# Kernel optimization log

Measured on AMD Instinct MI355X. Metric: run time of the kernel, lower is better.

Reference implementation:

```python
import jax, jax.numpy as jnp
import numpy as np

B, S, D, H, DFF, L, R, V = 2, 1024, 1024, 16, 4096, 2, 3, 32000
HD = D // H


def layer_norm(x, g, b, eps=1e-5):
    mu = jnp.mean(x, axis=-1, keepdims=True)
    var = jnp.var(x, axis=-1, keepdims=True)
    return (x - mu) / jnp.sqrt(var + eps) * g + b


def recursion_block(x, mask, Wqkv, bqkv, Wo, bo, W1, b1, W2, b2, ln1_g, ln1_b, ln2_g, ln2_b):
    # shared pre-LN transformer stack of L layers, applied once per recursion step
    Bc, Sc, _ = x.shape
    scale = 1.0 / np.sqrt(HD).astype(np.float32)
    for l in range(L):
        h = layer_norm(x, ln1_g[l], ln1_b[l])
        qkv = h @ Wqkv[l] + bqkv[l]
        q, k, v = jnp.split(qkv, 3, axis=-1)
        q = q.reshape(Bc, Sc, H, HD).transpose(0, 2, 1, 3)
        k = k.reshape(Bc, Sc, H, HD).transpose(0, 2, 1, 3)
        v = v.reshape(Bc, Sc, H, HD).transpose(0, 2, 1, 3)
        scores = jnp.einsum('bhqd,bhkd->bhqk', q, k) * scale + mask
        attn = jax.nn.softmax(scores, axis=-1)
        o = jnp.einsum('bhqk,bhkd->bhqd', attn, v).transpose(0, 2, 1, 3).reshape(Bc, Sc, D)
        x = x + o @ Wo[l] + bo[l]
        h2 = layer_norm(x, ln2_g[l], ln2_b[l])
        x = x + jax.nn.gelu(h2 @ W1[l] + b1[l]) @ W2[l] + b2[l]
    return x


def setup_inputs() -> dict:
    key = jax.random.key(0)
    ks = jax.random.split(key, 12)
    n = lambda k, shape: (jax.random.normal(k, shape, jnp.float32) * 0.02)
    return {
        'input_ids': jax.random.randint(ks[0], (B, S), 0, V),
        'token_embed': n(ks[1], (V, D)),
        'pos_embed': n(ks[2], (S, D)),
        'Wqkv': n(ks[3], (L, D, 3 * D)), 'bqkv': jnp.zeros((L, 3 * D), jnp.float32),
        'Wo': n(ks[4], (L, D, D)), 'bo': jnp.zeros((L, D), jnp.float32),
        'W1': n(ks[5], (L, D, DFF)), 'b1': jnp.zeros((L, DFF), jnp.float32),
        'W2': n(ks[6], (L, DFF, D)), 'b2': jnp.zeros((L, D), jnp.float32),
        'ln1_g': jnp.ones((L, D), jnp.float32), 'ln1_b': jnp.zeros((L, D), jnp.float32),
        'ln2_g': jnp.ones((L, D), jnp.float32), 'ln2_b': jnp.zeros((L, D), jnp.float32),
        'final_g': jnp.ones((D,), jnp.float32), 'final_b': jnp.zeros((D,), jnp.float32),
        'Wr': n(ks[7], (D, R)), 'br': jnp.zeros((R,), jnp.float32),
    }


def reference(input_ids, token_embed, pos_embed, Wqkv, bqkv, Wo, bo, W1, b1, W2, b2,
              ln1_g, ln1_b, ln2_g, ln2_b, final_g, final_b, Wr, br):
    h = token_embed[input_ids] + pos_embed[None, :, :]            # [B,S,D]
    mask = jnp.where(jnp.tril(jnp.ones((S, S), bool)), 0.0, -jnp.inf)[None, None]  # [1,1,S,S]
    # token-choice router on detached hidden states
    rlogits = jax.lax.stop_gradient(h) @ Wr + br                  # [B,S,R]
    probs = jax.nn.softmax(rlogits, axis=-1)
    depth_map = jnp.argmax(rlogits, axis=-1) + 1                  # depths in 1..R
    importance = probs.mean(axis=(0, 1))
    router_loss = R * jnp.sum(importance ** 2)                    # load-balance aux loss
    res = h
    for step in range(R):
        step_mask = depth_map >= step + 1                         # [B,S] bool
        upd = recursion_block(res, mask, Wqkv, bqkv, Wo, bo, W1, b1, W2, b2,
                              ln1_g, ln1_b, ln2_g, ln2_b)
        res = jnp.where(step_mask[..., None], upd, res)
    hf = layer_norm(res, final_g, final_b)
    logits = hf @ token_embed.T                                   # tied lm_head
    return logits, depth_map, router_loss
```

## Files before the change

kernel.cpp:

```cpp
#include <hip/hip_runtime.h>
#include <hip/hip_bf16.h>

#define DD 1024
#define SS 1024
#define BB 2
#define HH 16
#define DFFN 4096
#define LLAYERS 2
#define RSTEPS 3
#define VV 32000
#define NTOK (BB*SS)

typedef __attribute__((ext_vector_type(8))) short s16x8;
typedef __attribute__((ext_vector_type(8))) __bf16 bf16x8;
typedef __attribute__((ext_vector_type(4))) float f32x4;

__device__ __forceinline__ unsigned short f2bf(float f) {
  unsigned int u = __float_as_uint(f);
  u += 0x7FFFu + ((u >> 16) & 1u);
  return (unsigned short)(u >> 16);
}

__device__ __forceinline__ f32x4 mfma16(s16x8 a, s16x8 b, f32x4 c) {
  return __builtin_amdgcn_mfma_f32_16x16x32_bf16(
      __builtin_bit_cast(bf16x8, a), __builtin_bit_cast(bf16x8, b), c, 0, 0, 0);
}

__device__ __forceinline__ void gload16(const unsigned short* g, unsigned short* l) {
  __builtin_amdgcn_global_load_lds(
      (const __attribute__((address_space(1))) unsigned int*)(const void*)g,
      (__attribute__((address_space(3))) unsigned int*)(void*)l, 16, 0, 0);
}

#define BAR()  asm volatile("s_barrier" ::: "memory")
#define LGK0() do { asm volatile("s_waitcnt lgkmcnt(0)" ::: "memory"); \
                    __builtin_amdgcn_sched_barrier(0); } while (0)
#define VM4()  asm volatile("s_waitcnt vmcnt(4)" ::: "memory")
#define VM0()  asm volatile("s_waitcnt vmcnt(0)" ::: "memory")

__global__ __launch_bounds__(256) void wtrans_all_kernel(
    const float* __restrict__ Wqkv, const float* __restrict__ Wo,
    const float* __restrict__ W1, const float* __restrict__ W2,
    const float* __restrict__ te,
    unsigned short* __restrict__ WqkvT, unsigned short* __restrict__ WoT,
    unsigned short* __restrict__ W1T, unsigned short* __restrict__ W2T,
    unsigned short* __restrict__ teb) {
  const int bid = blockIdx.x;
  const int tid = threadIdx.x;
  if (bid >= 6144) {
    long i = ((long)(bid - 6144) * 256 + tid) * 8;
    float4 v0 = *(const float4*)(te + i);
    float4 v1 = *(const float4*)(te + i + 4);
    ushort4 a, b;
    a.x = f2bf(v0.x); a.y = f2bf(v0.y); a.z = f2bf(v0.z); a.w = f2bf(v0.w);
    b.x = f2bf(v1.x); b.y = f2bf(v1.y); b.z = f2bf(v1.z); b.w = f2bf(v1.w);
    *(ushort4*)(teb + i) = a;
    *(ushort4*)(teb + i + 4) = b;
    return;
  }
  const float* src; unsigned short* dst; int Kd, Nd, local;
  if (bid < 1536) {
    int l = (bid >= 768);
    local = bid - l * 768;
    src = Wqkv + (long)l * DD * 3 * DD; dst = WqkvT + (long)l * 3 * DD * DD;
    Kd = DD; Nd = 3 * DD;
  } else if (bid < 2048) {
    int l = (bid - 1536) >> 8; local = (bid - 1536) & 255;
    src = Wo + (long)l * DD * DD; dst = WoT + (long)l * DD * DD;
    Kd = DD; Nd = DD;
  } else if (bid < 4096) {
    int l = (bid - 2048) >> 10; local = (bid - 2048) & 1023;
    src = W1 + (long)l * DD * DFFN; dst = W1T + (long)l * DFFN * DD;
    Kd = DD; Nd = DFFN;
  } else {
    int l = (bid - 4096) >> 10; local = (bid - 4096) & 1023;
    src = W2 + (long)l * DFFN * DD; dst = W2T + (long)l * DD * DFFN;
    Kd = DFFN; Nd = DD;
  }
  const int tn = Nd >> 6;
  const int n0 = (local % tn) * 64, k0 = (local / tn) * 64;
  __shared__ unsigned short t[64][68];
#pragma unroll
  for (int c = 0; c < 4; ++c) {
    int p = tid + c * 256;
    int kr = p >> 4, nc = (p & 15) * 4;
    float4 v = *(const float4*)(src + (long)(k0 + kr) * Nd + n0 + nc);
    t[nc + 0][kr] = f2bf(v.x);
    t[nc + 1][kr] = f2bf(v.y);
    t[nc + 2][kr] = f2bf(v.z);
    t[nc + 3][kr] = f2bf(v.w);
  }
  __syncthreads();
#pragma unroll
  for (int c = 0; c < 4; ++c) {
    int p = tid + c * 256;
    int nr = p >> 4, kc = (p & 15) * 4;
    ushort4 o;
    o.x = t[nr][kc]; o.y = t[nr][kc + 1]; o.z = t[nr][kc + 2]; o.w = t[nr][kc + 3];
    *(ushort4*)(dst + (long)(n0 + nr) * Kd + k0 + kc) = o;
  }
}

__global__ __launch_bounds__(256) void embed_router_kernel(
    const int* __restrict__ ids, const float* __restrict__ te,
    const float* __restrict__ pe, const float* __restrict__ Wr,
    const float* __restrict__ br, float* __restrict__ res,
    float* __restrict__ probs, float* __restrict__ depth_ws,
    float* __restrict__ out_depth) {
  int row = blockIdx.x;
  int s = row & (SS - 1);
  int id = ids[row];
  int t = threadIdx.x;
  int d = t * 4;
  float4 a = *(const float4*)(te + (long)id * DD + d);
  float4 p = *(const float4*)(pe + (long)s * DD + d);
  float4 o; o.x = a.x + p.x; o.y = a.y + p.y; o.z = a.z + p.z; o.w = a.w + p.w;
  *(float4*)(res + (long)row * DD + d) = o;
  float a0 = 0.f, a1 = 0.f, a2 = 0.f;
  float hv[4] = {o.x, o.y, o.z, o.w};
#pragma unroll
  for (int j = 0; j < 4; ++j) {
    int dd = d + j;
    a0 += hv[j] * Wr[dd * 3 + 0];
    a1 += hv[j] * Wr[dd * 3 + 1];
    a2 += hv[j] * Wr[dd * 3 + 2];
  }
  for (int off = 32; off; off >>= 1) {
    a0 += __shfl_down(a0, off);
    a1 += __shfl_down(a1, off);
    a2 += __shfl_down(a2, off);
  }
  __shared__ float red[4][3];
  int wave = t >> 6;
  if ((t & 63) == 0) { red[wave][0] = a0; red[wave][1] = a1; red[wave][2] = a2; }
  __syncthreads();
  if (t == 0) {
    a0 = red[0][0] + red[1][0] + red[2][0] + red[3][0] + br[0];
    a1 = red[0][1] + red[1][1] + red[2][1] + red[3][1] + br[1];
    a2 = red[0][2] + red[1][2] + red[2][2] + red[3][2] + br[2];
    float m = fmaxf(a0, fmaxf(a1, a2));
    float e0 = expf(a0 - m), e1 = expf(a1 - m), e2 = expf(a2 - m);
    float inv = 1.f / (e0 + e1 + e2);
    probs[row * 3 + 0] = e0 * inv;
    probs[row * 3 + 1] = e1 * inv;
    probs[row * 3 + 2] = e2 * inv;
    int am = 0; float bv = a0;
    if (a1 > bv) { bv = a1; am = 1; }
    if (a2 > bv) { bv = a2; am = 2; }
    float dm = (float)(am + 1);
    depth_ws[row] = dm;
    out_depth[row] = dm;
  }
}

__global__ __launch_bounds__(256) void router_finalize_kernel(
    const float* __restrict__ probs, float* __restrict__ out_loss) {
  __shared__ float red[256][3];
  int t = threadIdx.x;
  float s0 = 0.f, s1 = 0.f, s2 = 0.f;
  for (int r = t; r < NTOK; r += 256) {
    s0 += probs[r * 3 + 0]; s1 += probs[r * 3 + 1]; s2 += probs[r * 3 + 2];
  }
  red[t][0] = s0; red[t][1] = s1; red[t][2] = s2;
  __syncthreads();
  for (int off = 128; off; off >>= 1) {
    if (t < off) {
      red[t][0] += red[t + off][0];
      red[t][1] += red[t + off][1];
      red[t][2] += red[t + off][2];
    }
    __syncthreads();
  }
  if (t == 0) {
    float i0 = red[0][0] / NTOK, i1 = red[0][1] / NTOK, i2 = red[0][2] / NTOK;
    out_loss[0] = (float)RSTEPS * (i0 * i0 + i1 * i1 + i2 * i2);
  }
}

__global__ __launch_bounds__(256) void ln_kernel(
    const float* __restrict__ x, const float* __restrict__ g,
    const float* __restrict__ b, unsigned short* __restrict__ y) {
  int row = blockIdx.x;
  int t = threadIdx.x;
  float4 v = *(const float4*)(x + (long)row * DD + t * 4);
  float s = v.x + v.y + v.z + v.w;
  float q = v.x * v.x + v.y * v.y + v.z * v.z + v.w * v.w;
  for (int off = 32; off; off >>= 1) {
    s += __shfl_down(s, off);
    q += __shfl_down(q, off);
  }
  __shared__ float rs[4], rq[4];
  int wave = t >> 6;
  if ((t & 63) == 0) { rs[wave] = s; rq[wave] = q; }
  __syncthreads();
  float S_ = rs[0] + rs[1] + rs[2] + rs[3];
  float Q_ = rq[0] + rq[1] + rq[2] + rq[3];
  float mu = S_ * (1.f / DD);
  float var = Q_ * (1.f / DD) - mu * mu;
  float rstd = rsqrtf(var + 1e-5f);
  int d = t * 4;
  float4 gg = *(const float4*)(g + d);
  float4 bb = *(const float4*)(b + d);
  ushort4 ov;
  ov.x = f2bf((v.x - mu) * rstd * gg.x + bb.x);
  ov.y = f2bf((v.y - mu) * rstd * gg.y + bb.y);
  ov.z = f2bf((v.z - mu) * rstd * gg.z + bb.z);
  ov.w = f2bf((v.w - mu) * rstd * gg.w + bb.w);
  *(ushort4*)(y + (long)row * DD + d) = ov;
}

__device__ __forceinline__ void stageA8(unsigned short* S, int buf, int qm,
    const unsigned short* A, int lda, long m0, int kt, int tid) {
  unsigned short* dst = S + buf * 32768 + qm * 8192;
#pragma unroll
  for (int c = 0; c < 2; ++c) {
    int idx = tid + c * 512;
    int L = (idx << 4) ^ (((idx >> 5) & 1) << 5);
    int band = L >> 13, row = (L >> 7) & 63, kel = (L & 127) >> 1;
    gload16(A + (m0 + band * 128 + qm * 64 + row) * (long)lda + kt * 64 + kel,
            dst + idx * 8);
  }
}

__device__ __forceinline__ void stageB8(unsigned short* S, int buf, int qn,
    const unsigned short* Bt, int ldb, long n0, int kt, int tid) {
  unsigned short* dst = S + buf * 32768 + 16384 + qn * 8192;
#pragma unroll
  for (int c = 0; c < 2; ++c) {
    int idx = tid + c * 512;
    int L = (idx << 4) ^ (((idx >> 5) & 1) << 5);
    int band = L >> 12, row = (L >> 7) & 31, kel = (L & 127) >> 1;
    gload16(Bt + (n0 + band * 64 + qn * 32 + row) * (long)ldb + kt * 64 + kel,
            dst + idx * 8);
  }
}

__device__ __forceinline__ void read_af8(const unsigned short* S, int base,
    int wm, int l16, int g, s16x8 af[2][4]) {
  const int swz = ((l16 >> 2) & 1) << 5;
#pragma unroll
  for (int kk = 0; kk < 2; ++kk)
#pragma unroll
    for (int mf = 0; mf < 4; ++mf) {
      int L = (wm * 8192 + (mf * 16 + l16) * 128 + (kk * 32 + g * 8) * 2) ^ swz;
      af[kk][mf] = *(const s16x8*)(S + base + (L >> 1));
    }
}

__device__ __forceinline__ void read_bf8(const unsigned short* S, int base,
    int wn, int l16, int g, s16x8 bf[2][2]) {
  const int swz = ((l16 >> 2) & 1) << 5;
#pragma unroll
  for (int kk = 0; kk < 2; ++kk)
#pragma unroll
    for (int nf = 0; nf < 2; ++nf) {
      int L = (wn * 4096 + (nf * 16 + l16) * 128 + (kk * 32 + g * 8) * 2) ^ swz;
      bf[kk][nf] = *(const s16x8*)(S + base + (L >> 1));
    }
}

template<int QM, int QN>
__device__ __forceinline__ void do_mfma8(f32x4 acc[8][4],
    const s16x8 af[2][4], const s16x8 bf[2][2]) {
  __builtin_amdgcn_s_setprio(1);
#pragma unroll
  for (int kk = 0; kk < 2; ++kk)
#pragma unroll
    for (int mf = 0; mf < 4; ++mf)
#pragma unroll
      for (int nf = 0; nf < 2; ++nf)
        acc[QM * 4 + mf][QN * 2 + nf] =
            mfma16(af[kk][mf], bf[kk][nf], acc[QM * 4 + mf][QN * 2 + nf]);
  __builtin_amdgcn_s_setprio(0);
}

template<int CBF16, int BIAS, int GELU_ACT>
__global__ __launch_bounds__(512, 1) void gemm256_kernel(
    const unsigned short* __restrict__ A, int lda,
    const unsigned short* __restrict__ Bt, int ldb,
    void* __restrict__ Cv, int ldc,
    const float* __restrict__ bias, int K, int Mblocks) {
  __shared__ unsigned short S[65536];
  const int tid = threadIdx.x;
  const int lane = tid & 63, wave = tid >> 6;
  const int g = lane >> 4, l16 = lane & 15;
  const int wm = wave >> 2, wn = wave & 3;
  const int nwg = gridDim.x * gridDim.y;
  const int orig = blockIdx.x + blockIdx.y * gridDim.x;
  const int q = nwg >> 3, r = nwg & 7;
  const int xcd = orig & 7, loc = orig >> 3;
  const int wgid = (xcd < r ? xcd * (q + 1) : r * (q + 1) + (xcd - r) * q) + loc;
  const long m0 = (long)(wgid % Mblocks) * 256;
  const long n0 = (long)(wgid / Mblocks) * 256;

  f32x4 acc[8][4] = {};
  s16x8 af[2][4], bf[2][2];
  const int NI = K >> 7;

  stageA8(S, 0, 0, A, lda, m0, 0, tid);
  stageA8(S, 0, 1, A, lda, m0, 0, tid);
  stageB8(S, 0, 0, Bt, ldb, n0, 0, tid);
  stageB8(S, 0, 1, Bt, ldb, n0, 0, tid);
  stageA8(S, 1, 0, A, lda, m0, 1, tid);
  stageB8(S, 1, 1, Bt, ldb, n0, 1, tid);
  VM4(); BAR();

  for (int i = 0; i < NI; ++i) {
    const int kt1 = 2 * i + 1, kt2 = 2 * i + 2, kt3 = 2 * i + 3;
    const bool more = (i + 1 < NI);
    read_af8(S, 0, wm, l16, g, af);
    read_bf8(S, 16384, wn, l16, g, bf);
    stageA8(S, 1, 1, A, lda, m0, kt1, tid);
    BAR(); LGK0();
    do_mfma8<0, 0>(acc, af, bf);
    BAR();
    read_bf8(S, 16384 + 8192, wn, l16, g, bf);
    stageB8(S, 1, 0, Bt, ldb, n0, kt1, tid);
    BAR(); LGK0();
    do_mfma8<0, 1>(acc, af, bf);
    BAR();
    read_af8(S, 8192, wm, l16, g, af);
    if (more) stageA8(S, 0, 0, A, lda, m0, kt2, tid);
    BAR(); LGK0();
    do_mfma8<1, 1>(acc, af, bf);
    BAR();
    read_bf8(S, 16384, wn, l16, g, bf);
    if (more) stageB8(S, 0, 1, Bt, ldb, n0, kt2, tid);
    BAR(); LGK0();
    do_mfma8<1, 0>(acc, af, bf);
    if (more) { VM4(); } else { VM0(); }
    BAR();
    read_af8(S, 32768, wm, l16, g, af);
    read_bf8(S, 32768 + 16384, wn, l16, g, bf);
    if (more) stageA8(S, 0, 1, A, lda, m0, kt2, tid);
    BAR(); LGK0();
    do_mfma8<0, 0>(acc, af, bf);
    BAR();
    read_bf8(S, 32768 + 16384 + 8192, wn, l16, g, bf);
    if (more) stageB8(S, 0, 0, Bt, ldb, n0, kt2, tid);
    BAR(); LGK0();
    do_mfma8<0, 1>(acc, af, bf);
    BAR();
    read_af8(S, 32768 + 8192, wm, l16, g, af);
    if (more) stageA8(S, 1, 0, A, lda, m0, kt3, tid);
    BAR(); LGK0();
    do_mfma8<1, 1>(acc, af, bf);
    BAR();
    read_bf8(S, 32768 + 16384, wn, l16, g, bf);
    if (more) stageB8(S, 1, 1, Bt, ldb, n0, kt3, tid);
    BAR(); LGK0();
    do_mfma8<1, 0>(acc, af, bf);
    VM4(); BAR();
  }

#pragma unroll
  for (int mf = 0; mf < 8; ++mf) {
#pragma unroll
    for (int nf = 0; nf < 4; ++nf) {
      long row0 = m0 + wm * 128 + mf * 16 + g * 4;
      long col = n0 + wn * 64 + nf * 16 + l16;
      float bv = BIAS ? bias[col] : 0.f;
#pragma unroll
      for (int rr = 0; rr < 4; ++rr) {
        float v = acc[mf][nf][rr] + bv;
        if (GELU_ACT) {
          float x3 = v * v * v;
          v = 0.5f * v * (1.f + tanhf(0.7978845608028654f * (v + 0.044715f * x3)));
        }
        if (CBF16) ((unsigned short*)Cv)[(row0 + rr) * (long)ldc + col] = f2bf(v);
        else       ((float*)Cv)[(row0 + rr) * (long)ldc + col] = v;
      }
    }
  }
}

template<int BN, int CBF16, int BIAS, int RESID, int GELU_ACT, int SELW, int QKVW>
__global__ __launch_bounds__(256) void gemm128_kernel(
    const unsigned short* __restrict__ A, int lda,
    const unsigned short* __restrict__ Bt, int ldb,
    void* __restrict__ Cv, int ldc,
    const float* __restrict__ bias,
    const float* __restrict__ resid, int ldr,
    const float* __restrict__ depth_ws, float stepf,
    unsigned short* __restrict__ vtw,
    int K) {
  constexpr int BM = 128;
  constexpr int WN = BN / 2;
  constexpr int MR = 4;
  constexpr int NR = WN / 16;
  __shared__ unsigned short As[BM * 64];
  __shared__ unsigned short Bs[BN * 64];
  const int tid = threadIdx.x;
  const int lane = tid & 63, wave = tid >> 6;
  const int g = lane >> 4, l16 = lane & 15;
  const int wr = wave >> 1, wc = wave & 1;
  int lin = blockIdx.x + blockIdx.y * gridDim.x;
  int per = (gridDim.x * gridDim.y) >> 3;
  int v = (lin & 7) * per + (lin >> 3);
  const long m0 = (long)(v % gridDim.y) * BM;
  const long n0 = (long)(v / gridDim.y) * BN;
  f32x4 acc[MR][NR] = {};
  for (int k0 = 0; k0 < K; k0 += 64) {
    __syncthreads();
#pragma unroll
    for (int c = 0; c < BM / 32; ++c) {
      int p = tid + c * 256;
      int r = p >> 3, kq = (p & 7) * 8;
      gload16(A + (m0 + r) * (long)lda + k0 + kq, &As[p * 8]);
    }
#pragma unroll
    for (int c = 0; c < BN / 32; ++c) {
      int p = tid + c * 256;
      int r = p >> 3, kq = (p & 7) * 8;
      gload16(Bt + (n0 + r) * (long)ldb + k0 + kq, &Bs[p * 8]);
    }
    __syncthreads();
#pragma unroll
    for (int kk = 0; kk < 2; ++kk) {
      s16x8 af[MR], bf[NR];
#pragma unroll
      for (int m = 0; m < MR; ++m)
        af[m] = *(const s16x8*)&As[(wr * 64 + m * 16 + l16) * 64 + kk * 32 + g * 8];
#pragma unroll
      for (int n = 0; n < NR; ++n)
        bf[n] = *(const s16x8*)&Bs[(wc * WN + n * 16 + l16) * 64 + kk * 32 + g * 8];
#pragma unroll
      for (int m = 0; m < MR; ++m)
#pragma unroll
        for (int n = 0; n < NR; ++n)
          acc[m][n] = mfma16(af[m], bf[n], acc[m][n]);
    }
  }
  const bool vblk = QKVW && (n0 >= 2048);
#pragma unroll
  for (int m = 0; m < MR; ++m) {
#pragma unroll
    for (int n = 0; n < NR; ++n) {
      long row_base = m0 + wr * 64 + m * 16 + g * 4;
      long col = n0 + wc * WN + n * 16 + l16;
      float bv = BIAS ? bias[col] : 0.f;
      float vv4[4];
#pragma unroll
      for (int r = 0; r < 4; ++r) {
        long row = row_base + r;
        float vv = acc[m][n][r] + bv;
        if (RESID) vv += resid[row * (long)ldr + col];
        if (GELU_ACT) {
          float x3 = vv * vv * vv;
          vv = 0.5f * vv * (1.f + tanhf(0.7978845608028654f * (vv + 0.044715f * x3)));
        }
        vv4[r] = vv;
      }
      if (QKVW && vblk) {
        int rel = (int)col - 2048;
        int h = rel >> 6, d = rel & 63;
        int b = (int)(row_base >> 10);
        int s = (int)(row_base & 1023);
        ushort4 o;
        o.x = f2bf(vv4[0]); o.y = f2bf(vv4[1]);
        o.z = f2bf(vv4[2]); o.w = f2bf(vv4[3]);
        *(ushort4*)(vtw + (((long)(b * 16 + h) * 64 + d) * SS + s)) = o;
      } else {
#pragma unroll
        for (int r = 0; r < 4; ++r) {
          long row = row_base + r;
          if (SELW) {
            if (depth_ws[row] >= stepf)
              ((float*)Cv)[row * (long)ldc + col] = vv4[r];
          } else if (CBF16) {
            ((unsigned short*)Cv)[row * (long)ldc + col] = f2bf(vv4[r]);
          } else {
            ((float*)Cv)[row * (long)ldc + col] = vv4[r];
          }
        }
      }
    }
  }
}

__global__ __launch_bounds__(512) void attn_kernel(
    const unsigned short* __restrict__ qkv,
    const unsigned short* __restrict__ vt,
    unsigned short* __restrict__ o) {
  __shared__ unsigned short Ks[2][64 * 64];
  __shared__ unsigned short Vs[2][64 * 64];
  __shared__ unsigned short Pl[8][16][72];
  const int qb = blockIdx.x;
  const int bh = blockIdx.y;
  const int b = bh >> 4, h = bh & 15;
  const int tid = threadIdx.x, wave = tid >> 6, lane = tid & 63;
  const int g = lane >> 4, l16 = lane & 15;
  const float NEG_INF = -__builtin_inff();
  const int q0 = qb * 128;
  const int qrw = q0 + wave * 16;
  const long rowbase = (long)b * SS;
  const unsigned short* kbase = qkv + rowbase * 3072 + 1024 + h * 64;
  const unsigned short* vbase = vt + (long)bh * 64 * SS;

  const unsigned short* qptr = qkv + (rowbase + qrw + l16) * 3072 + h * 64;
  s16x8 qf0 = *(const s16x8*)(qptr + g * 8);
  s16x8 qf1 = *(const s16x8*)(qptr + 32 + g * 8);

  f32x4 oacc[4] = {};
  float mrun = NEG_INF, lrun = 0.f;

  const int ntile = q0 / 64 + 2;

  {
    int r = tid >> 3;
    int bo = (tid & 7) * 16;
    int sw = (bo ^ ((r & 7) << 4)) >> 1;
    gload16(kbase + (long)r * 3072 + sw, &Ks[0][tid * 8]);
    gload16(vbase + (long)r * SS + 0 + sw, &Vs[0][tid * 8]);
  }
  asm volatile("s_waitcnt vmcnt(0)" ::: "memory");
  __syncthreads();

  for (int t = 0; t < ntile; ++t) {
    const int cur = t & 1;
    const int kv0 = t * 64;
    const unsigned short* ks_cur = &Ks[cur][0];
    const unsigned short* vs_cur = &Vs[cur][0];
    if (t + 1 < ntile) {
      const int kvn = kv0 + 64;
      int r = tid >> 3;
      int bo = (tid & 7) * 16;
      int sw = (bo ^ ((r & 7) << 4)) >> 1;
      gload16(kbase + (long)(kvn + r) * 3072 + sw, &Ks[cur ^ 1][tid * 8]);
      gload16(vbase + (long)r * SS + kvn + sw, &Vs[cur ^ 1][tid * 8]);
    }
    f32x4 accs[4] = {};
#pragma unroll
    for (int ks = 0; ks < 2; ++ks) {
#pragma unroll
      for (int kvb = 0; kvb < 4; ++kvb) {
        int row = kvb * 16 + l16;
        int bo = ((ks * 64 + g * 16) ^ ((l16 & 7) << 4)) >> 1;
        s16x8 kf = *(const s16x8*)&ks_cur[row * 64 + bo];
        accs[kvb] = mfma16(kf, ks ? qf1 : qf0, accs[kvb]);
      }
    }
    const bool needmask = (kv0 + 63 > qrw);
    const int qabs = qrw + l16;
    float sv[4][4];
    float mloc = NEG_INF;
#pragma unroll
    for (int kvb = 0; kvb < 4; ++kvb) {
#pragma unroll
      for (int r = 0; r < 4; ++r) {
        float vv = accs[kvb][r] * 0.125f;
        if (needmask) {
          int kva = kv0 + kvb * 16 + g * 4 + r;
          if (kva > qabs) vv = NEG_INF;
        }
        sv[kvb][r] = vv;
        mloc = fmaxf(mloc, vv);
      }
    }
    mloc = fmaxf(mloc, __shfl_xor(mloc, 16));
    mloc = fmaxf(mloc, __shfl_xor(mloc, 32));
    float mnew = fmaxf(mrun, mloc);
    float alpha = __expf(mrun - mnew);
    float lsum = 0.f;
#pragma unroll
    for (int kvb = 0; kvb < 4; ++kvb) {
      float p0 = __expf(sv[kvb][0] - mnew);
      float p1 = __expf(sv[kvb][1] - mnew);
      float p2 = __expf(sv[kvb][2] - mnew);
      float p3 = __expf(sv[kvb][3] - mnew);
      lsum += (p0 + p1) + (p2 + p3);
      unsigned int w0 = (unsigned)f2bf(p0) | ((unsigned)f2bf(p1) << 16);
      unsigned int w1 = (unsigned)f2bf(p2) | ((unsigned)f2bf(p3) << 16);
      uint2 pw; pw.x = w0; pw.y = w1;
      *(uint2*)&Pl[wave][l16][kvb * 16 + g * 4] = pw;
    }
    lsum += __shfl_xor(lsum, 16);
    lsum += __shfl_xor(lsum, 32);
    lrun = lrun * alpha + lsum;
    mrun = mnew;
    float mult[4];
#pragma unroll
    for (int r = 0; r < 4; ++r) mult[r] = __shfl(alpha, g * 4 + r);
#pragma unroll
    for (int nd = 0; nd < 4; ++nd)
#pragma unroll
      for (int r = 0; r < 4; ++r) oacc[nd][r] *= mult[r];
#pragma unroll
    for (int kh = 0; kh < 2; ++kh) {
      s16x8 pa = *(const s16x8*)&Pl[wave][l16][kh * 32 + g * 8];
#pragma unroll
      for (int nd = 0; nd < 4; ++nd) {
        int row = nd * 16 + l16;
        int bo = ((kh * 64 + g * 16) ^ ((l16 & 7) << 4)) >> 1;
        s16x8 vf = *(const s16x8*)&vs_cur[row * 64 + bo];
        oacc[nd] = mfma16(pa, vf, oacc[nd]);
      }
    }
    asm volatile("s_waitcnt vmcnt(0)" ::: "memory");
    __syncthreads();
  }
  unsigned short* ob = o + (rowbase + qrw) * 1024 + h * 64;
#pragma unroll
  for (int r = 0; r < 4; ++r) {
    float lr = __shfl(lrun, g * 4 + r);
    float inv = 1.f / lr;
#pragma unroll
    for (int nd = 0; nd < 4; ++nd)
      ob[(long)(g * 4 + r) * 1024 + nd * 16 + l16] = f2bf(oacc[nd][r] * inv);
  }
}

extern "C" void kernel_launch(void* const* d_in, const int* in_sizes, int n_in,
                              void* d_out, int out_size, void* d_ws, size_t ws_size,
                              hipStream_t stream) {
  (void)in_sizes; (void)n_in; (void)out_size; (void)ws_size;
  const int*   ids  = (const int*)d_in[0];
  const float* te   = (const float*)d_in[1];
  const float* pe   = (const float*)d_in[2];
  const float* Wqkv = (const float*)d_in[3];
  const float* bqkv = (const float*)d_in[4];
  const float* Wo   = (const float*)d_in[5];
  const float* bo   = (const float*)d_in[6];
  const float* W1   = (const float*)d_in[7];
  const float* b1   = (const float*)d_in[8];
  const float* W2   = (const float*)d_in[9];
  const float* b2   = (const float*)d_in[10];
  const float* ln1g = (const float*)d_in[11];
  const float* ln1b = (const float*)d_in[12];
  const float* ln2g = (const float*)d_in[13];
  const float* ln2b = (const float*)d_in[14];
  const float* fing = (const float*)d_in[15];
  const float* finb = (const float*)d_in[16];
  const float* Wr   = (const float*)d_in[17];
  const float* br   = (const float*)d_in[18];

  float* logits    = (float*)d_out;
  float* out_depth = logits + (long)NTOK * VV;
  float* out_loss  = out_depth + NTOK;

  char* w = (char*)d_ws;
  float* res            = (float*)w;          w += (long)NTOK * DD * 4;
  float* x              = (float*)w;          w += (long)NTOK * DD * 4;
  unsigned short* hbuf  = (unsigned short*)w; w += (long)NTOK * DD * 2;
  unsigned short* qkvb  = (unsigned short*)w; w += (long)NTOK * 3 * DD * 2;
  unsigned short* obuf  = (unsigned short*)w; w += (long)NTOK * DD * 2;
  unsigned short* ffn1  = (unsigned short*)w; w += (long)NTOK * DFFN * 2;
  unsigned short* vtb   = (unsigned short*)w; w += (long)BB * HH * 64 * SS * 2;
  float* probs          = (float*)w;          w += (long)NTOK * 3 * 4;
  float* depth_ws       = (float*)w;          w += (long)NTOK * 4;
  unsigned short* WqkvT = (unsigned short*)w; w += (long)LLAYERS * 3 * DD * DD * 2;
  unsigned short* WoT   = (unsigned short*)w; w += (long)LLAYERS * DD * DD * 2;
  unsigned short* W1T   = (unsigned short*)w; w += (long)LLAYERS * DFFN * DD * 2;
  unsigned short* W2T   = (unsigned short*)w; w += (long)LLAYERS * DD * DFFN * 2;
  unsigned short* teb   = (unsigned short*)w; w += (long)VV * DD * 2;

  wtrans_all_kernel<<<6144 + 16000, 256, 0, stream>>>(
      Wqkv, Wo, W1, W2, te, WqkvT, WoT, W1T, W2T, teb);

  embed_router_kernel<<<NTOK, 256, 0, stream>>>(ids, te, pe, Wr, br,
                                                res, probs, depth_ws, out_depth);
  router_finalize_kernel<<<1, 256, 0, stream>>>(probs, out_loss);

  for (int step = 0; step < RSTEPS; ++step) {
    for (int l = 0; l < LLAYERS; ++l) {
      const float* xin = (l == 0) ? res : x;
      ln_kernel<<<NTOK, 256, 0, stream>>>(xin, ln1g + l * DD, ln1b + l * DD, hbuf);
      gemm128_kernel<128, 1, 1, 0, 0, 0, 1><<<dim3(3 * DD / 128, NTOK / 128), 256, 0, stream>>>(
          hbuf, DD, WqkvT + (long)l * 3 * DD * DD, DD, qkvb, 3 * DD,
          bqkv + (long)l * 3 * DD, nullptr, 0, nullptr, 0.f, vtb, DD);
      attn_kernel<<<dim3(SS / 128, BB * HH), 512, 0, stream>>>(qkvb, vtb, obuf);
      gemm128_kernel<64, 0, 1, 1, 0, 0, 0><<<dim3(DD / 64, NTOK / 128), 256, 0, stream>>>(
          obuf, DD, WoT + (long)l * DD * DD, DD, x, DD,
          bo + (long)l * DD, xin, DD, nullptr, 0.f, nullptr, DD);
      ln_kernel<<<NTOK, 256, 0, stream>>>(x, ln2g + l * DD, ln2b + l * DD, hbuf);
      gemm128_kernel<128, 1, 1, 0, 1, 0, 0><<<dim3(DFFN / 128, NTOK / 128), 256, 0, stream>>>(
          hbuf, DD, W1T + (long)l * DFFN * DD, DD, ffn1, DFFN,
          b1 + (long)l * DFFN, nullptr, 0, nullptr, 0.f, nullptr, DD);
      if (l == 0) {
        gemm128_kernel<64, 0, 1, 1, 0, 0, 0><<<dim3(DD / 64, NTOK / 128), 256, 0, stream>>>(
            ffn1, DFFN, W2T + (long)l * DD * DFFN, DFFN, x, DD,
            b2 + (long)l * DD, x, DD, nullptr, 0.f, nullptr, DFFN);
      } else {
        gemm128_kernel<64, 0, 1, 1, 0, 1, 0><<<dim3(DD / 64, NTOK / 128), 256, 0, stream>>>(
            ffn1, DFFN, W2T + (long)l * DD * DFFN, DFFN, res, DD,
            b2 + (long)l * DD, x, DD, depth_ws, (float)(step + 1), nullptr, DFFN);
      }
    }
  }
  ln_kernel<<<NTOK, 256, 0, stream>>>(res, fing, finb, hbuf);
  gemm256_kernel<0, 0, 0><<<dim3(VV / 256, NTOK / 256), 512, 0, stream>>>(
      hbuf, DD, teb, DD, logits, VV, nullptr, DD, NTOK / 256);
}
```

Before: 1.437 ms.

## Stage fp32 GEMM epilogue through LDS and read attention K/V directly from global

In the large GEMM kernel, the fp32-output epilogue now writes accumulators to a swizzled LDS tile one half at a time, then stores to global as coalesced float4 rows instead of scattered scalar stores. Separately, the attention kernel is reduced to 64-query blocks with 4 waves and drops the double-buffered LDS staging of K and V. Each wave now loads its K and V fragments straight from global or cache. This gives twice as many attention blocks with finer causal granularity, and removes LDS traffic and barriers from the attention loop. In exchange, K/V reuse across waves now depends on the cache, and the GEMM epilogue gains extra barriers.

```diff
diff --git a/kernel.cpp b/kernel.cpp
--- a/kernel.cpp
+++ b/kernel.cpp
@@ -353,23 +353,62 @@
     VM4(); BAR();
   }
 
-#pragma unroll
-  for (int mf = 0; mf < 8; ++mf) {
-#pragma unroll
-    for (int nf = 0; nf < 4; ++nf) {
-      long row0 = m0 + wm * 128 + mf * 16 + g * 4;
-      long col = n0 + wn * 64 + nf * 16 + l16;
-      float bv = BIAS ? bias[col] : 0.f;
-#pragma unroll
-      for (int rr = 0; rr < 4; ++rr) {
-        float v = acc[mf][nf][rr] + bv;
-        if (GELU_ACT) {
-          float x3 = v * v * v;
-          v = 0.5f * v * (1.f + tanhf(0.7978845608028654f * (v + 0.044715f * x3)));
+  if (CBF16) {
+#pragma unroll
+    for (int mf = 0; mf < 8; ++mf) {
+#pragma unroll
+      for (int nf = 0; nf < 4; ++nf) {
+        long row0 = m0 + wm * 128 + mf * 16 + g * 4;
+        long col = n0 + wn * 64 + nf * 16 + l16;
+        float bv = BIAS ? bias[col] : 0.f;
+#pragma unroll
+        for (int rr = 0; rr < 4; ++rr) {
+          float v = acc[mf][nf][rr] + bv;
+          if (GELU_ACT) {
+            float x3 = v * v * v;
+            v = 0.5f * v * (1.f + tanhf(0.7978845608028654f * (v + 0.044715f * x3)));
+          }
+          ((unsigned short*)Cv)[(row0 + rr) * (long)ldc + col] = f2bf(v);
         }
-        if (CBF16) ((unsigned short*)Cv)[(row0 + rr) * (long)ldc + col] = f2bf(v);
-        else       ((float*)Cv)[(row0 + rr) * (long)ldc + col] = v;
-      }
+      }
+    }
+  } else {
+    float* Sf = (float*)S;
+    float* Cf = (float*)Cv;
+#pragma unroll
+    for (int p = 0; p < 2; ++p) {
+      if (wm == p) {
+#pragma unroll
+        for (int mf = 0; mf < 8; ++mf) {
+#pragma unroll
+          for (int nf = 0; nf < 4; ++nf) {
+            int colw = wn * 64 + nf * 16 + l16;
+            float bv = BIAS ? bias[n0 + colw] : 0.f;
+#pragma unroll
+            for (int rr = 0; rr < 4; ++rr) {
+              int row = mf * 16 + g * 4 + rr;
+              float v = acc[mf][nf][rr] + bv;
+              if (GELU_ACT) {
+                float x3 = v * v * v;
+                v = 0.5f * v * (1.f + tanhf(0.7978845608028654f * (v + 0.044715f * x3)));
+              }
+              int fidx = ((row << 8) + colw) ^ (((row >> 2) & 3) << 4);
+              Sf[fidx] = v;
+            }
+          }
+        }
+      }
+      BAR();
+#pragma unroll
+      for (int c = 0; c < 16; ++c) {
+        int idx = tid + c * 512;
+        int row = idx >> 6, f4 = (idx & 63) << 2;
+        int fidx = ((row << 8) + f4) ^ (((row >> 2) & 3) << 4);
+        float4 v = *(const float4*)&Sf[fidx];
+        long rg = m0 + p * 128 + row;
+        *(float4*)(Cf + rg * (long)ldc + n0 + f4) = v;
+      }
+      BAR();
     }
   }
 }
@@ -478,20 +517,18 @@
   }
 }
 
-__global__ __launch_bounds__(512) void attn_kernel(
+__global__ __launch_bounds__(256) void attn_kernel(
     const unsigned short* __restrict__ qkv,
     const unsigned short* __restrict__ vt,
     unsigned short* __restrict__ o) {
-  __shared__ unsigned short Ks[2][64 * 64];
-  __shared__ unsigned short Vs[2][64 * 64];
-  __shared__ unsigned short Pl[8][16][72];
+  __shared__ unsigned short Pl[4][16][72];
   const int qb = blockIdx.x;
   const int bh = blockIdx.y;
   const int b = bh >> 4, h = bh & 15;
   const int tid = threadIdx.x, wave = tid >> 6, lane = tid & 63;
   const int g = lane >> 4, l16 = lane & 15;
   const float NEG_INF = -__builtin_inff();
-  const int q0 = qb * 128;
+  const int q0 = qb * 64;
   const int qrw = q0 + wave * 16;
   const long rowbase = (long)b * SS;
   const unsigned short* kbase = qkv + rowbase * 3072 + 1024 + h * 64;
@@ -504,39 +541,17 @@
   f32x4 oacc[4] = {};
   float mrun = NEG_INF, lrun = 0.f;
 
-  const int ntile = q0 / 64 + 2;
-
-  {
-    int r = tid >> 3;
-    int bo = (tid & 7) * 16;
-    int sw = (bo ^ ((r & 7) << 4)) >> 1;
-    gload16(kbase + (long)r * 3072 + sw, &Ks[0][tid * 8]);
-    gload16(vbase + (long)r * SS + 0 + sw, &Vs[0][tid * 8]);
-  }
-  asm volatile("s_waitcnt vmcnt(0)" ::: "memory");
-  __syncthreads();
-
+  const int ntile = q0 / 64 + 1;
   for (int t = 0; t < ntile; ++t) {
-    const int cur = t & 1;
     const int kv0 = t * 64;
-    const unsigned short* ks_cur = &Ks[cur][0];
-    const unsigned short* vs_cur = &Vs[cur][0];
-    if (t + 1 < ntile) {
-      const int kvn = kv0 + 64;
-      int r = tid >> 3;
-      int bo = (tid & 7) * 16;
-      int sw = (bo ^ ((r & 7) << 4)) >> 1;
-      gload16(kbase + (long)(kvn + r) * 3072 + sw, &Ks[cur ^ 1][tid * 8]);
-      gload16(vbase + (long)r * SS + kvn + sw, &Vs[cur ^ 1][tid * 8]);
-    }
     f32x4 accs[4] = {};
 #pragma unroll
     for (int ks = 0; ks < 2; ++ks) {
 #pragma unroll
       for (int kvb = 0; kvb < 4; ++kvb) {
-        int row = kvb * 16 + l16;
-        int bo = ((ks * 64 + g * 16) ^ ((l16 & 7) << 4)) >> 1;
-        s16x8 kf = *(const s16x8*)&ks_cur[row * 64 + bo];
+        const unsigned short* kp =
+            kbase + (long)(kv0 + kvb * 16 + l16) * 3072 + ks * 32 + g * 8;
+        s16x8 kf = *(const s16x8*)kp;
         accs[kvb] = mfma16(kf, ks ? qf1 : qf0, accs[kvb]);
       }
     }
@@ -590,14 +605,12 @@
       s16x8 pa = *(const s16x8*)&Pl[wave][l16][kh * 32 + g * 8];
 #pragma unroll
       for (int nd = 0; nd < 4; ++nd) {
-        int row = nd * 16 + l16;
-        int bo = ((kh * 64 + g * 16) ^ ((l16 & 7) << 4)) >> 1;
-        s16x8 vf = *(const s16x8*)&vs_cur[row * 64 + bo];
+        const unsigned short* vp =
+            vbase + (long)(nd * 16 + l16) * SS + kv0 + kh * 32 + g * 8;
+        s16x8 vf = *(const s16x8*)vp;
         oacc[nd] = mfma16(pa, vf, oacc[nd]);
       }
     }
-    asm volatile("s_waitcnt vmcnt(0)" ::: "memory");
-    __syncthreads();
   }
   unsigned short* ob = o + (rowbase + qrw) * 1024 + h * 64;
 #pragma unroll
@@ -668,7 +681,7 @@
       gemm128_kernel<128, 1, 1, 0, 0, 0, 1><<<dim3(3 * DD / 128, NTOK / 128), 256, 0, stream>>>(
           hbuf, DD, WqkvT + (long)l * 3 * DD * DD, DD, qkvb, 3 * DD,
           bqkv + (long)l * 3 * DD, nullptr, 0, nullptr, 0.f, vtb, DD);
-      attn_kernel<<<dim3(SS / 128, BB * HH), 512, 0, stream>>>(qkvb, vtb, obuf);
+      attn_kernel<<<dim3(SS / 64, BB * HH), 256, 0, stream>>>(qkvb, vtb, obuf);
       gemm128_kernel<64, 0, 1, 1, 0, 0, 0><<<dim3(DD / 64, NTOK / 128), 256, 0, stream>>>(
           obuf, DD, WoT + (long)l * DD * DD, DD, x, DD,
           bo + (long)l * DD, xin, DD, nullptr, 0.f, nullptr, DD);
```

Result: slower. 1.609 ms (+12.0%).
